# Performance work log

Hardware: AMD Instinct MI355X
Metric: run time of the kernel (lower is better)

Reference implementation:

```python
import jax, jax.numpy as jnp
import numpy as np

N_NODES = 200000
N_EDGES = 4000000

# SE3 layout (pypose convention): [tx, ty, tz, qx, qy, qz, qw]

def _qmul(q, r):
    x1, y1, z1, w1 = q[..., 0], q[..., 1], q[..., 2], q[..., 3]
    x2, y2, z2, w2 = r[..., 0], r[..., 1], r[..., 2], r[..., 3]
    return jnp.stack([
        w1 * x2 + x1 * w2 + y1 * z2 - z1 * y2,
        w1 * y2 - x1 * z2 + y1 * w2 + z1 * x2,
        w1 * z2 + x1 * y2 - y1 * x2 + z1 * w2,
        w1 * w2 - x1 * x2 - y1 * y2 - z1 * z2,
    ], axis=-1)


def _qrot(q, v):
    # rotate vector v by unit quaternion q: v + w*t + qv x t, t = 2 qv x v
    qv, w = q[..., :3], q[..., 3:4]
    t = 2.0 * jnp.cross(qv, v)
    return v + w * t + jnp.cross(qv, t)


def _se3_inv(T):
    t, q = T[..., :3], T[..., 3:]
    qi = q * jnp.asarray([-1.0, -1.0, -1.0, 1.0], dtype=T.dtype)
    ti = -_qrot(qi, t)
    return jnp.concatenate([ti, qi], axis=-1)


def _se3_mul(T1, T2):
    t1, q1 = T1[..., :3], T1[..., 3:]
    t2, q2 = T2[..., :3], T2[..., 3:]
    return jnp.concatenate([t1 + _qrot(q1, t2), _qmul(q1, q2)], axis=-1)


def _se3_log(T):
    # SE3 Log -> se3 [rho(3), phi(3)] (pypose order: translational part first)
    t, q = T[..., :3], T[..., 3:]
    # canonicalize quaternion to w >= 0 (shortest rotation)
    q = jnp.where(q[..., 3:4] < 0, -q, q)
    qv, w = q[..., :3], q[..., 3]
    n = jnp.linalg.norm(qv, axis=-1)           # sin(theta/2)
    theta = 2.0 * jnp.arctan2(n, w)            # rotation angle in [0, pi]
    small = n < 1e-6
    safe_n = jnp.where(small, 1.0, n)
    # phi = theta * axis ; small-angle: 2/w (Taylor of 2*atan2(n,w)/n)
    scale = jnp.where(small, 2.0 / jnp.maximum(w, 1e-12), theta / safe_n)
    phi = scale[..., None] * qv
    # rho = Jl(phi)^{-1} t
    th2 = theta * theta
    tiny = theta < 1e-4
    safe_th = jnp.where(tiny, 1.0, theta)
    coef = jnp.where(
        tiny,
        1.0 / 12.0 + th2 / 720.0,
        1.0 / jnp.where(tiny, 1.0, th2)
        - (1.0 + jnp.cos(safe_th)) / (2.0 * safe_th * jnp.sin(safe_th)),
    )
    pxt = jnp.cross(phi, t)
    rho = t - 0.5 * pxt + coef[..., None] * jnp.cross(phi, pxt)
    return jnp.concatenate([rho, phi], axis=-1)


def _random_se3(key, n):
    kt, kq = jax.random.split(key)
    t = jax.random.normal(kt, (n, 3), dtype=jnp.float32)
    q = jax.random.normal(kq, (n, 4), dtype=jnp.float32)
    q = q / jnp.linalg.norm(q, axis=-1, keepdims=True)
    return jnp.concatenate([t, q], axis=-1)


def setup_inputs() -> dict:
    key = jax.random.key(0)
    k1, k2, k3 = jax.random.split(key, 3)
    nodes = _random_se3(k1, N_NODES)            # [N, 7]
    poses = _random_se3(k2, N_EDGES)            # [E, 7]
    edges = jax.random.randint(k3, (N_EDGES, 2), 0, N_NODES, dtype=jnp.int64)
    return {"nodes": nodes, "poses": poses, "edges": edges}


def reference(nodes, poses, edges):
    node1 = nodes[edges[..., 0]]                # [E, 7] gather
    node2 = nodes[edges[..., 1]]                # [E, 7] gather
    error = _se3_mul(_se3_mul(poses, _se3_inv(node1)), node2)
    return _se3_log(error)                      # [E, 6]
```

## Files before the change

kernel.cpp:

```cpp
#include <hip/hip_runtime.h>

constexpr int BLK = 256;

struct F3 { float x, y, z; };
struct F4 { float x, y, z, w; };

__device__ inline F3 cross3(const F3 a, const F3 b) {
    return { a.y * b.z - a.z * b.y,
             a.z * b.x - a.x * b.z,
             a.x * b.y - a.y * b.x };
}

__device__ inline F3 qrot(const F4 q, const F3 v) {
    F3 qv{ q.x, q.y, q.z };
    F3 t = cross3(qv, v);
    t.x *= 2.f; t.y *= 2.f; t.z *= 2.f;
    F3 c = cross3(qv, t);
    return { v.x + q.w * t.x + c.x,
             v.y + q.w * t.y + c.y,
             v.z + q.w * t.z + c.z };
}

__device__ inline F4 qmul(const F4 a, const F4 b) {
    return { a.w * b.x + a.x * b.w + a.y * b.z - a.z * b.y,
             a.w * b.y - a.x * b.z + a.y * b.w + a.z * b.x,
             a.w * b.z + a.x * b.y - a.y * b.x + a.z * b.w,
             a.w * b.w - a.x * b.x - a.y * b.y - a.z * b.z };
}

__global__ __launch_bounds__(BLK) void pose_graph_err_kernel(
    const float* __restrict__ nodes,
    const float* __restrict__ poses,
    const int*   __restrict__ edges,
    float*       __restrict__ out,
    int n_edges)
{
    __shared__ float s_pose[BLK * 7];
    __shared__ float s_out [BLK * 6];

    const int tid = threadIdx.x;
    const int block_start = blockIdx.x * BLK;
    const int cnt = min(BLK, n_edges - block_start);

    if (cnt == BLK) {
        const float4* pv = (const float4*)(poses + (size_t)block_start * 7);
        float4* sp = (float4*)s_pose;
        #pragma unroll
        for (int i = tid; i < BLK * 7 / 4; i += BLK) sp[i] = pv[i];
    } else {
        for (int i = tid; i < cnt * 7; i += BLK)
            s_pose[i] = poses[(size_t)block_start * 7 + i];
    }
    __syncthreads();

    F3 rho{0.f,0.f,0.f}, phi{0.f,0.f,0.f};
    const int e = block_start + tid;
    if (tid < cnt) {
        const float* sp = s_pose + tid * 7;
        F3 tp{ sp[0], sp[1], sp[2] };
        F4 qp{ sp[3], sp[4], sp[5], sp[6] };

        const int2 ij = ((const int2*)edges)[e];
        const float* n1 = nodes + (size_t)ij.x * 7;
        const float* n2 = nodes + (size_t)ij.y * 7;

        F3 t1{ n1[0], n1[1], n1[2] };
        F4 q1{ n1[3], n1[4], n1[5], n1[6] };
        F3 t2{ n2[0], n2[1], n2[2] };
        F4 q2{ n2[3], n2[4], n2[5], n2[6] };

        F4 qi{ -q1.x, -q1.y, -q1.z, q1.w };
        F3 ti = qrot(qi, t1);
        ti.x = -ti.x; ti.y = -ti.y; ti.z = -ti.z;

        F3 ra = qrot(qp, ti);
        F3 tA{ tp.x + ra.x, tp.y + ra.y, tp.z + ra.z };
        F4 qA = qmul(qp, qi);

        F3 rb = qrot(qA, t2);
        F3 tE{ tA.x + rb.x, tA.y + rb.y, tA.z + rb.z };
        F4 qE = qmul(qA, q2);

        if (qE.w < 0.f) { qE.x = -qE.x; qE.y = -qE.y; qE.z = -qE.z; qE.w = -qE.w; }
        const float n2q = qE.x * qE.x + qE.y * qE.y + qE.z * qE.z;
        const float nq = sqrtf(n2q);
        const float theta = 2.f * atan2f(nq, qE.w);
        const bool small = nq < 1e-6f;
        const float scale = small ? (2.f / fmaxf(qE.w, 1e-12f)) : (theta / nq);
        phi = { scale * qE.x, scale * qE.y, scale * qE.z };

        const float th2 = theta * theta;
        const bool tiny = theta < 1e-4f;
        float coef;
        if (tiny) {
            coef = 1.f / 12.f + th2 / 720.f;
        } else {
            coef = 1.f / th2 - (1.f + cosf(theta)) / (2.f * theta * sinf(theta));
        }

        const F3 pxt  = cross3(phi, tE);
        const F3 ppxt = cross3(phi, pxt);
        rho = { tE.x - 0.5f * pxt.x + coef * ppxt.x,
                tE.y - 0.5f * pxt.y + coef * ppxt.y,
                tE.z - 0.5f * pxt.z + coef * ppxt.z };

        float* so = s_out + tid * 6;
        so[0] = rho.x; so[1] = rho.y; so[2] = rho.z;
        so[3] = phi.x; so[4] = phi.y; so[5] = phi.z;
    }
    __syncthreads();

    if (cnt == BLK) {
        float4* ov = (float4*)(out + (size_t)block_start * 6);
        const float4* sv = (const float4*)s_out;
        #pragma unroll
        for (int i = tid; i < BLK * 6 / 4; i += BLK) ov[i] = sv[i];
    } else {
        for (int i = tid; i < cnt * 6; i += BLK)
            out[(size_t)block_start * 6 + i] = s_out[i];
    }
}

extern "C" void kernel_launch(void* const* d_in, const int* in_sizes, int n_in,
                              void* d_out, int out_size, void* d_ws, size_t ws_size,
                              hipStream_t stream) {
    const float* nodes = (const float*)d_in[0];
    const float* poses = (const float*)d_in[1];
    const int*   edges = (const int*)d_in[2];
    float* out = (float*)d_out;

    const int n_edges = in_sizes[2] / 2;
    const int nblocks = (n_edges + BLK - 1) / BLK;
    pose_graph_err_kernel<<<nblocks, BLK, 0, stream>>>(nodes, poses, edges, out, n_edges);
}
```

Baseline: 105.7 us.

## Process four edges per thread with direct vector loads, dropping shared staging

Each thread now handles four consecutive edges. It loads their poses (28 floats) as seven float4 and their indices as two int4 directly from global memory. All eight node gathers are issued before any compute, and the results go out as six float4 stores. This removes shared-memory staging and the two block barriers, and gives more memory-level parallelism per thread. In exchange, per-thread float4 accesses stride 112 bytes across lanes, which hurts coalescing, and register pressure rises, which may lower occupancy.

New measurement: 140.7 us. +33.1%, slower.

```diff
diff --git a/kernel.cpp b/kernel.cpp
--- a/kernel.cpp
+++ b/kernel.cpp
@@ -1,17 +1,18 @@
 #include <hip/hip_runtime.h>
 
 constexpr int BLK = 256;
+constexpr int EPT = 4;
 
 struct F3 { float x, y, z; };
 struct F4 { float x, y, z, w; };
 
-__device__ inline F3 cross3(const F3 a, const F3 b) {
+__device__ __forceinline__ F3 cross3(const F3 a, const F3 b) {
     return { a.y * b.z - a.z * b.y,
              a.z * b.x - a.x * b.z,
              a.x * b.y - a.y * b.x };
 }
 
-__device__ inline F3 qrot(const F4 q, const F3 v) {
+__device__ __forceinline__ F3 qrot(const F4 q, const F3 v) {
     F3 qv{ q.x, q.y, q.z };
     F3 t = cross3(qv, v);
     t.x *= 2.f; t.y *= 2.f; t.z *= 2.f;
@@ -21,11 +22,57 @@
              v.z + q.w * t.z + c.z };
 }
 
-__device__ inline F4 qmul(const F4 a, const F4 b) {
+__device__ __forceinline__ F4 qmul(const F4 a, const F4 b) {
     return { a.w * b.x + a.x * b.w + a.y * b.z - a.z * b.y,
              a.w * b.y - a.x * b.z + a.y * b.w + a.z * b.x,
              a.w * b.z + a.x * b.y - a.y * b.x + a.z * b.w,
              a.w * b.w - a.x * b.x - a.y * b.y - a.z * b.z };
+}
+
+__device__ __forceinline__ void edge_compute(const F3 tp, const F4 qp,
+                                             const float* __restrict__ n1,
+                                             const float* __restrict__ n2,
+                                             float* __restrict__ o)
+{
+    F3 t1{ n1[0], n1[1], n1[2] };
+    F4 q1{ n1[3], n1[4], n1[5], n1[6] };
+    F3 t2{ n2[0], n2[1], n2[2] };
+    F4 q2{ n2[3], n2[4], n2[5], n2[6] };
+
+    F4 qi{ -q1.x, -q1.y, -q1.z, q1.w };
+    F3 ti = qrot(qi, t1);
+    ti.x = -ti.x; ti.y = -ti.y; ti.z = -ti.z;
+
+    F3 ra = qrot(qp, ti);
+    F3 tA{ tp.x + ra.x, tp.y + ra.y, tp.z + ra.z };
+    F4 qA = qmul(qp, qi);
+
+    F3 rb = qrot(qA, t2);
+    F3 tE{ tA.x + rb.x, tA.y + rb.y, tA.z + rb.z };
+    F4 qE = qmul(qA, q2);
+
+    if (qE.w < 0.f) { qE.x = -qE.x; qE.y = -qE.y; qE.z = -qE.z; qE.w = -qE.w; }
+    const float n2q = qE.x * qE.x + qE.y * qE.y + qE.z * qE.z;
+    const float nq = sqrtf(n2q);
+    const float theta = 2.f * atan2f(nq, qE.w);
+    const bool small = nq < 1e-6f;
+    const float scale = small ? (2.f / fmaxf(qE.w, 1e-12f)) : (theta / nq);
+    const F3 phi{ scale * qE.x, scale * qE.y, scale * qE.z };
+
+    const float th2 = theta * theta;
+    float coef;
+    if (theta < 1e-4f) {
+        coef = 1.f / 12.f + th2 / 720.f;
+    } else {
+        coef = 1.f / th2 - (1.f + cosf(theta)) / (2.f * theta * sinf(theta));
+    }
+
+    const F3 pxt  = cross3(phi, tE);
+    const F3 ppxt = cross3(phi, pxt);
+    o[0] = tE.x - 0.5f * pxt.x + coef * ppxt.x;
+    o[1] = tE.y - 0.5f * pxt.y + coef * ppxt.y;
+    o[2] = tE.z - 0.5f * pxt.z + coef * ppxt.z;
+    o[3] = phi.x; o[4] = phi.y; o[5] = phi.z;
 }
 
 __global__ __launch_bounds__(BLK) void pose_graph_err_kernel(
@@ -35,89 +82,50 @@
     float*       __restrict__ out,
     int n_edges)
 {
-    __shared__ float s_pose[BLK * 7];
-    __shared__ float s_out [BLK * 6];
+    const long long t  = (long long)blockIdx.x * BLK + threadIdx.x;
+    const long long e0 = t * EPT;
+    if (e0 >= n_edges) return;
 
-    const int tid = threadIdx.x;
-    const int block_start = blockIdx.x * BLK;
-    const int cnt = min(BLK, n_edges - block_start);
+    if (e0 + EPT <= (long long)n_edges) {
+        union { float4 v[7]; float f[28]; } P;
+        const float4* pv = (const float4*)(poses + e0 * 7);
+        #pragma unroll
+        for (int j = 0; j < 7; ++j) P.v[j] = pv[j];
 
-    if (cnt == BLK) {
-        const float4* pv = (const float4*)(poses + (size_t)block_start * 7);
-        float4* sp = (float4*)s_pose;
+        union { int4 v[2]; int i[8]; } E;
+        const int4* ev = (const int4*)(edges + e0 * 2);
+        E.v[0] = ev[0]; E.v[1] = ev[1];
+
+        float nd[8][7];
         #pragma unroll
-        for (int i = tid; i < BLK * 7 / 4; i += BLK) sp[i] = pv[i];
-    } else {
-        for (int i = tid; i < cnt * 7; i += BLK)
-            s_pose[i] = poses[(size_t)block_start * 7 + i];
-    }
-    __syncthreads();
-
-    F3 rho{0.f,0.f,0.f}, phi{0.f,0.f,0.f};
-    const int e = block_start + tid;
-    if (tid < cnt) {
-        const float* sp = s_pose + tid * 7;
-        F3 tp{ sp[0], sp[1], sp[2] };
-        F4 qp{ sp[3], sp[4], sp[5], sp[6] };
-
-        const int2 ij = ((const int2*)edges)[e];
-        const float* n1 = nodes + (size_t)ij.x * 7;
-        const float* n2 = nodes + (size_t)ij.y * 7;
-
-        F3 t1{ n1[0], n1[1], n1[2] };
-        F4 q1{ n1[3], n1[4], n1[5], n1[6] };
-        F3 t2{ n2[0], n2[1], n2[2] };
-        F4 q2{ n2[3], n2[4], n2[5], n2[6] };
-
-        F4 qi{ -q1.x, -q1.y, -q1.z, q1.w };
-        F3 ti = qrot(qi, t1);
-        ti.x = -ti.x; ti.y = -ti.y; ti.z = -ti.z;
-
-        F3 ra = qrot(qp, ti);
-        F3 tA{ tp.x + ra.x, tp.y + ra.y, tp.z + ra.z };
-        F4 qA = qmul(qp, qi);
-
-        F3 rb = qrot(qA, t2);
-        F3 tE{ tA.x + rb.x, tA.y + rb.y, tA.z + rb.z };
-        F4 qE = qmul(qA, q2);
-
-        if (qE.w < 0.f) { qE.x = -qE.x; qE.y = -qE.y; qE.z = -qE.z; qE.w = -qE.w; }
-        const float n2q = qE.x * qE.x + qE.y * qE.y + qE.z * qE.z;
-        const float nq = sqrtf(n2q);
-        const float theta = 2.f * atan2f(nq, qE.w);
-        const bool small = nq < 1e-6f;
-        const float scale = small ? (2.f / fmaxf(qE.w, 1e-12f)) : (theta / nq);
-        phi = { scale * qE.x, scale * qE.y, scale * qE.z };
-
-        const float th2 = theta * theta;
-        const bool tiny = theta < 1e-4f;
-        float coef;
-        if (tiny) {
-            coef = 1.f / 12.f + th2 / 720.f;
-        } else {
-            coef = 1.f / th2 - (1.f + cosf(theta)) / (2.f * theta * sinf(theta));
+        for (int k = 0; k < 8; ++k) {
+            const float* np = nodes + (size_t)E.i[k] * 7;
+            #pragma unroll
+            for (int j = 0; j < 7; ++j) nd[k][j] = np[j];
         }
 
-        const F3 pxt  = cross3(phi, tE);
-        const F3 ppxt = cross3(phi, pxt);
-        rho = { tE.x - 0.5f * pxt.x + coef * ppxt.x,
-                tE.y - 0.5f * pxt.y + coef * ppxt.y,
-                tE.z - 0.5f * pxt.z + coef * ppxt.z };
+        union { float4 v[6]; float f[24]; } O;
+        #pragma unroll
+        for (int k = 0; k < EPT; ++k) {
+            F3 tp{ P.f[k*7+0], P.f[k*7+1], P.f[k*7+2] };
+            F4 qp{ P.f[k*7+3], P.f[k*7+4], P.f[k*7+5], P.f[k*7+6] };
+            edge_compute(tp, qp, nd[2*k], nd[2*k+1], &O.f[k*6]);
+        }
 
-        float* so = s_out + tid * 6;
-        so[0] = rho.x; so[1] = rho.y; so[2] = rho.z;
-        so[3] = phi.x; so[4] = phi.y; so[5] = phi.z;
-    }
-    __syncthreads();
-
-    if (cnt == BLK) {
-        float4* ov = (float4*)(out + (size_t)block_start * 6);
-        const float4* sv = (const float4*)s_out;
+        float4* ov = (float4*)(out + e0 * 6);
         #pragma unroll
-        for (int i = tid; i < BLK * 6 / 4; i += BLK) ov[i] = sv[i];
+        for (int j = 0; j < 6; ++j) ov[j] = O.v[j];
     } else {
-        for (int i = tid; i < cnt * 6; i += BLK)
-            out[(size_t)block_start * 6 + i] = s_out[i];
+        for (long long e = e0; e < (long long)n_edges; ++e) {
+            const float* sp = poses + e * 7;
+            F3 tp{ sp[0], sp[1], sp[2] };
+            F4 qp{ sp[3], sp[4], sp[5], sp[6] };
+            const int i1 = edges[e*2], i2 = edges[e*2+1];
+            float o[6];
+            edge_compute(tp, qp, nodes + (size_t)i1 * 7, nodes + (size_t)i2 * 7, o);
+            #pragma unroll
+            for (int j = 0; j < 6; ++j) out[e*6+j] = o[j];
+        }
     }
 }
 
@@ -130,6 +138,7 @@
     float* out = (float*)d_out;
 
     const int n_edges = in_sizes[2] / 2;
-    const int nblocks = (n_edges + BLK - 1) / BLK;
+    const int per_block = BLK * EPT;
+    const int nblocks = (n_edges + per_block - 1) / per_block;
     pose_graph_err_kernel<<<nblocks, BLK, 0, stream>>>(nodes, poses, edges, out, n_edges);
 }
```

## Drop shared-memory staging; use per-thread nontemporal loads/stores and simplify log coefficient

Applied to the files above, without the earlier changes.

Removes the LDS staging of poses and outputs along with both block barriers. Each thread now reads its own 7 pose floats and its edge pair with nontemporal loads, and writes its 6 outputs as three nontemporal 2-float stores. The log coefficient drops the cos/sin evaluation and uses the identity (1+cos)/(2 theta sin) = w/(2 theta n), which is valid for the half-angle quaternion. The risk is uncoalesced strided per-thread access in place of the previous coalesced float4 block copies.

Result: slower. 141.1 us (+33.4%).

```diff
diff --git a/kernel.cpp b/kernel.cpp
--- a/kernel.cpp
+++ b/kernel.cpp
@@ -1,17 +1,20 @@
 #include <hip/hip_runtime.h>
+
+typedef float vf2 __attribute__((ext_vector_type(2)));
+typedef int   vi2 __attribute__((ext_vector_type(2)));
 
 constexpr int BLK = 256;
 
 struct F3 { float x, y, z; };
 struct F4 { float x, y, z, w; };
 
-__device__ inline F3 cross3(const F3 a, const F3 b) {
+__device__ __forceinline__ F3 cross3(const F3 a, const F3 b) {
     return { a.y * b.z - a.z * b.y,
              a.z * b.x - a.x * b.z,
              a.x * b.y - a.y * b.x };
 }
 
-__device__ inline F3 qrot(const F4 q, const F3 v) {
+__device__ __forceinline__ F3 qrot(const F4 q, const F3 v) {
     F3 qv{ q.x, q.y, q.z };
     F3 t = cross3(qv, v);
     t.x *= 2.f; t.y *= 2.f; t.z *= 2.f;
@@ -21,7 +24,7 @@
              v.z + q.w * t.z + c.z };
 }
 
-__device__ inline F4 qmul(const F4 a, const F4 b) {
+__device__ __forceinline__ F4 qmul(const F4 a, const F4 b) {
     return { a.w * b.x + a.x * b.w + a.y * b.z - a.z * b.y,
              a.w * b.y - a.x * b.z + a.y * b.w + a.z * b.x,
              a.w * b.z + a.x * b.y - a.y * b.x + a.z * b.w,
@@ -35,90 +38,70 @@
     float*       __restrict__ out,
     int n_edges)
 {
-    __shared__ float s_pose[BLK * 7];
-    __shared__ float s_out [BLK * 6];
+    const long long e = (long long)blockIdx.x * BLK + threadIdx.x;
+    if (e >= n_edges) return;
 
-    const int tid = threadIdx.x;
-    const int block_start = blockIdx.x * BLK;
-    const int cnt = min(BLK, n_edges - block_start);
+    const vi2 ij = __builtin_nontemporal_load((const vi2*)edges + e);
 
-    if (cnt == BLK) {
-        const float4* pv = (const float4*)(poses + (size_t)block_start * 7);
-        float4* sp = (float4*)s_pose;
-        #pragma unroll
-        for (int i = tid; i < BLK * 7 / 4; i += BLK) sp[i] = pv[i];
-    } else {
-        for (int i = tid; i < cnt * 7; i += BLK)
-            s_pose[i] = poses[(size_t)block_start * 7 + i];
-    }
-    __syncthreads();
+    float p[7];
+    const float* pp = poses + e * 7;
+    #pragma unroll
+    for (int j = 0; j < 7; ++j) p[j] = __builtin_nontemporal_load(pp + j);
 
-    F3 rho{0.f,0.f,0.f}, phi{0.f,0.f,0.f};
-    const int e = block_start + tid;
-    if (tid < cnt) {
-        const float* sp = s_pose + tid * 7;
-        F3 tp{ sp[0], sp[1], sp[2] };
-        F4 qp{ sp[3], sp[4], sp[5], sp[6] };
+    const float* g1 = nodes + (size_t)ij.x * 7;
+    const float* g2 = nodes + (size_t)ij.y * 7;
+    float n1[7], n2[7];
+    #pragma unroll
+    for (int j = 0; j < 7; ++j) n1[j] = g1[j];
+    #pragma unroll
+    for (int j = 0; j < 7; ++j) n2[j] = g2[j];
 
-        const int2 ij = ((const int2*)edges)[e];
-        const float* n1 = nodes + (size_t)ij.x * 7;
-        const float* n2 = nodes + (size_t)ij.y * 7;
+    const F3 tp{ p[0], p[1], p[2] };
+    const F4 qp{ p[3], p[4], p[5], p[6] };
+    const F3 t1{ n1[0], n1[1], n1[2] };
+    const F4 q1{ n1[3], n1[4], n1[5], n1[6] };
+    const F3 t2{ n2[0], n2[1], n2[2] };
+    const F4 q2{ n2[3], n2[4], n2[5], n2[6] };
 
-        F3 t1{ n1[0], n1[1], n1[2] };
-        F4 q1{ n1[3], n1[4], n1[5], n1[6] };
-        F3 t2{ n2[0], n2[1], n2[2] };
-        F4 q2{ n2[3], n2[4], n2[5], n2[6] };
+    const F4 qi{ -q1.x, -q1.y, -q1.z, q1.w };
+    F3 ti = qrot(qi, t1);
+    ti.x = -ti.x; ti.y = -ti.y; ti.z = -ti.z;
 
-        F4 qi{ -q1.x, -q1.y, -q1.z, q1.w };
-        F3 ti = qrot(qi, t1);
-        ti.x = -ti.x; ti.y = -ti.y; ti.z = -ti.z;
+    const F3 ra = qrot(qp, ti);
+    const F3 tA{ tp.x + ra.x, tp.y + ra.y, tp.z + ra.z };
+    const F4 qA = qmul(qp, qi);
 
-        F3 ra = qrot(qp, ti);
-        F3 tA{ tp.x + ra.x, tp.y + ra.y, tp.z + ra.z };
-        F4 qA = qmul(qp, qi);
+    const F3 rb = qrot(qA, t2);
+    const F3 tE{ tA.x + rb.x, tA.y + rb.y, tA.z + rb.z };
+    F4 qE = qmul(qA, q2);
 
-        F3 rb = qrot(qA, t2);
-        F3 tE{ tA.x + rb.x, tA.y + rb.y, tA.z + rb.z };
-        F4 qE = qmul(qA, q2);
+    const float sflip = (qE.w < 0.f) ? -1.f : 1.f;
+    qE.x *= sflip; qE.y *= sflip; qE.z *= sflip; qE.w *= sflip;
 
-        if (qE.w < 0.f) { qE.x = -qE.x; qE.y = -qE.y; qE.z = -qE.z; qE.w = -qE.w; }
-        const float n2q = qE.x * qE.x + qE.y * qE.y + qE.z * qE.z;
-        const float nq = sqrtf(n2q);
-        const float theta = 2.f * atan2f(nq, qE.w);
-        const bool small = nq < 1e-6f;
-        const float scale = small ? (2.f / fmaxf(qE.w, 1e-12f)) : (theta / nq);
-        phi = { scale * qE.x, scale * qE.y, scale * qE.z };
+    const float n2q = qE.x * qE.x + qE.y * qE.y + qE.z * qE.z;
+    const float nq = sqrtf(n2q);
+    const float theta = 2.f * atan2f(nq, qE.w);
 
-        const float th2 = theta * theta;
-        const bool tiny = theta < 1e-4f;
-        float coef;
-        if (tiny) {
-            coef = 1.f / 12.f + th2 / 720.f;
-        } else {
-            coef = 1.f / th2 - (1.f + cosf(theta)) / (2.f * theta * sinf(theta));
-        }
+    const float scale = (nq < 1e-6f) ? (2.f / fmaxf(qE.w, 1e-12f)) : (theta / nq);
+    const F3 phi{ scale * qE.x, scale * qE.y, scale * qE.z };
 
-        const F3 pxt  = cross3(phi, tE);
-        const F3 ppxt = cross3(phi, pxt);
-        rho = { tE.x - 0.5f * pxt.x + coef * ppxt.x,
-                tE.y - 0.5f * pxt.y + coef * ppxt.y,
-                tE.z - 0.5f * pxt.z + coef * ppxt.z };
+    const float th2 = theta * theta;
+    const float coef = (theta < 1e-4f)
+        ? (1.f / 12.f + th2 / 720.f)
+        : (1.f / th2 - qE.w / (2.f * theta * nq));
 
-        float* so = s_out + tid * 6;
-        so[0] = rho.x; so[1] = rho.y; so[2] = rho.z;
-        so[3] = phi.x; so[4] = phi.y; so[5] = phi.z;
-    }
-    __syncthreads();
+    const F3 pxt  = cross3(phi, tE);
+    const F3 ppxt = cross3(phi, pxt);
 
-    if (cnt == BLK) {
-        float4* ov = (float4*)(out + (size_t)block_start * 6);
-        const float4* sv = (const float4*)s_out;
-        #pragma unroll
-        for (int i = tid; i < BLK * 6 / 4; i += BLK) ov[i] = sv[i];
-    } else {
-        for (int i = tid; i < cnt * 6; i += BLK)
-            out[(size_t)block_start * 6 + i] = s_out[i];
-    }
+    vf2* ov = (vf2*)(out + e * 6);
+    vf2 o0{ tE.x - 0.5f * pxt.x + coef * ppxt.x,
+            tE.y - 0.5f * pxt.y + coef * ppxt.y };
+    vf2 o1{ tE.z - 0.5f * pxt.z + coef * ppxt.z,
+            phi.x };
+    vf2 o2{ phi.y, phi.z };
+    __builtin_nontemporal_store(o0, ov + 0);
+    __builtin_nontemporal_store(o1, ov + 1);
+    __builtin_nontemporal_store(o2, ov + 2);
 }
 
 extern "C" void kernel_launch(void* const* d_in, const int* in_sizes, int n_in,
```
